# Kernel optimization log

Measured on AMD Instinct MI355X. Metric: run time of the kernel, lower is better.

The kernel has to match this reference:

```python
import jax, jax.numpy as jnp
import numpy as np
import math

N, D, H, E, ED = 2048, 256, 8, 65536, 64
HD = D // H  # head_dim = 32


def _layernorm(x, g, b, eps=1e-5):
    mu = jnp.mean(x, axis=-1, keepdims=True)
    var = jnp.mean((x - mu) ** 2, axis=-1, keepdims=True)
    return (x - mu) * jax.lax.rsqrt(var + eps) * g + b


def setup_inputs() -> dict:
    key = jax.random.key(0)
    ks = jax.random.split(key, 24)
    s = 0.02
    inp = {
        "x": jax.random.normal(ks[0], (N, D), jnp.float32),
        "edge_index": jax.random.randint(ks[1], (2, E), 0, N, jnp.int64),
        "edge_attr": jax.random.normal(ks[2], (E, ED), jnp.float32),
        # attention projections (stored [in, out]; y = x @ W + b)
        "Wq": jax.random.normal(ks[3], (D, D), jnp.float32) * s,
        "bq": jnp.zeros((D,), jnp.float32),
        "Wk": jax.random.normal(ks[4], (D, D), jnp.float32) * s,
        "bk": jnp.zeros((D,), jnp.float32),
        "Wv": jax.random.normal(ks[5], (D, D), jnp.float32) * s,
        "bv": jnp.zeros((D,), jnp.float32),
        "Wo": jax.random.normal(ks[6], (D, D), jnp.float32) * s,
        "bo": jnp.zeros((D,), jnp.float32),
        # edge bias projection: edge_dim -> num_heads
        "We": jax.random.normal(ks[7], (ED, H), jnp.float32) * s,
        "be": jnp.zeros((H,), jnp.float32),
        # FFN
        "W1": jax.random.normal(ks[8], (D, 4 * D), jnp.float32) * s,
        "b1": jnp.zeros((4 * D,), jnp.float32),
        "W2": jax.random.normal(ks[9], (4 * D, D), jnp.float32) * s,
        "b2": jnp.zeros((D,), jnp.float32),
        # layernorms
        "ln1_g": jnp.ones((D,), jnp.float32),
        "ln1_b": jnp.zeros((D,), jnp.float32),
        "ln2_g": jnp.ones((D,), jnp.float32),
        "ln2_b": jnp.zeros((D,), jnp.float32),
    }
    return inp


def reference(x, edge_index, edge_attr, Wq, bq, Wk, bk, Wv, bv, Wo, bo,
              We, be, W1, b1, W2, b2, ln1_g, ln1_b, ln2_g, ln2_b):
    n = x.shape[0]
    scale = math.sqrt(HD)
    src, dst = edge_index[0], edge_index[1]

    residual = x
    h = _layernorm(x, ln1_g, ln1_b)
    Q = (h @ Wq + bq).reshape(n, H, HD)
    K = (h @ Wk + bk).reshape(n, H, HD)
    V = (h @ Wv + bv).reshape(n, H, HD)

    # dense [N, N, H] scores, matching the original einsum
    scores = jnp.einsum('nhd,mhd->nmh', Q, K) / scale

    # adjacency mask with self-loops (scatter .set semantics, like torch assignment)
    diag = jnp.arange(n)
    adj = jnp.zeros((n, n), jnp.bool_).at[src, dst].set(True)
    adj = adj.at[diag, diag].set(True)

    # edge bias scattered into [N, N, H] (assignment semantics)
    edge_bias = edge_attr @ We + be  # [E, H]
    bias = jnp.zeros((n, n, H), scores.dtype).at[src, dst].set(edge_bias)
    scores = scores + bias

    scores = jnp.where(adj[:, :, None], scores, -jnp.inf)
    # softmax over dim=1 (source/key nodes m)
    attn = jax.nn.softmax(scores, axis=1)

    out = jnp.einsum('nmh,mhd->nhd', attn, V).reshape(n, D)
    out = out @ Wo + bo
    x = residual + out

    residual = x
    h2 = _layernorm(x, ln2_g, ln2_b)
    ffn = jax.nn.gelu(h2 @ W1 + b1, approximate=False) @ W2 + b2
    return residual + ffn
```

## Files before the change

### kernel.cpp

```cpp
#include <hip/hip_runtime.h>
#include <math.h>

#define D 256
#define NH 8
#define HD 32
#define EDIM 64

typedef __attribute__((ext_vector_type(8))) short bfrag;
typedef __attribute__((ext_vector_type(4))) float ffrag;

__device__ __forceinline__ unsigned short f2bf(float x) {
  unsigned int u = __float_as_uint(x);
  return (unsigned short)((u + 0x7FFFu + ((u >> 16) & 1u)) >> 16);
}

__global__ __launch_bounds__(256) void ln_kernel(const float* __restrict__ x,
    const float* __restrict__ g, const float* __restrict__ b,
    unsigned short* __restrict__ out) {
  int row = blockIdx.x;
  int tid = threadIdx.x;
  float v = x[row * D + tid];
  float s = v, sq = v * v;
  #pragma unroll
  for (int m = 1; m < 64; m <<= 1) { s += __shfl_xor(s, m); sq += __shfl_xor(sq, m); }
  __shared__ float ps[4], pq[4];
  int wid = tid >> 6, lane = tid & 63;
  if (lane == 0) { ps[wid] = s; pq[wid] = sq; }
  __syncthreads();
  float ts = ps[0] + ps[1] + ps[2] + ps[3];
  float tq = pq[0] + pq[1] + pq[2] + pq[3];
  float mu  = ts * (1.f / D);
  float var = tq * (1.f / D) - mu * mu;
  float inv = 1.f / sqrtf(var + 1e-5f);
  out[row * D + tid] = f2bf((v - mu) * inv * g[tid] + b[tid]);
}

__global__ __launch_bounds__(256) void cast6_kernel(
    const float* __restrict__ s0, const float* __restrict__ s1,
    const float* __restrict__ s2, const float* __restrict__ s3,
    const float* __restrict__ s4, const float* __restrict__ s5,
    unsigned short* __restrict__ d0, unsigned short* __restrict__ d1,
    unsigned short* __restrict__ d2, unsigned short* __restrict__ d3,
    unsigned short* __restrict__ d4, unsigned short* __restrict__ d5) {
  int i = (blockIdx.x * 256 + threadIdx.x) * 4;
  const float* s; unsigned short* d; int off;
  if      (i < 65536)  { s = s0; d = d0; off = i; }
  else if (i < 131072) { s = s1; d = d1; off = i - 65536; }
  else if (i < 196608) { s = s2; d = d2; off = i - 131072; }
  else if (i < 262144) { s = s3; d = d3; off = i - 196608; }
  else if (i < 524288) { s = s4; d = d4; off = i - 262144; }
  else if (i < 786432) { s = s5; d = d5; off = i - 524288; }
  else return;
  float4 v = *(const float4*)(s + off);
  ushort4 o = make_ushort4(f2bf(v.x), f2bf(v.y), f2bf(v.z), f2bf(v.w));
  *(ushort4*)(d + off) = o;
}

__device__ __forceinline__ void mg_core(const unsigned short* __restrict__ A,
    const unsigned short* __restrict__ B, int K, int Nn, int bm, int bn,
    int kb0, int kb1, unsigned short (*As)[40], unsigned short (*Bt)[40],
    ffrag acc[4]) {
  int tid = threadIdx.x;
  int wid = tid >> 6, lane = tid & 63;
  int lr = lane & 15, lk = lane >> 4;
  int ar = tid >> 2, ak = (tid & 3) * 8;
  int bnn = tid & 63, bkg = tid >> 6;
  for (int kb = kb0; kb < kb1; kb += 32) {
    uint4 av = *(const uint4*)(A + (size_t)(bm + ar) * K + kb + ak);
    *(uint4*)&As[ar][ak] = av;
    unsigned int u[4];
    #pragma unroll
    for (int jj = 0; jj < 4; jj++) {
      unsigned short lo = B[(size_t)(kb + bkg * 8 + 2 * jj)     * Nn + bn + bnn];
      unsigned short hi = B[(size_t)(kb + bkg * 8 + 2 * jj + 1) * Nn + bn + bnn];
      u[jj] = (unsigned int)lo | ((unsigned int)hi << 16);
    }
    *(uint4*)&Bt[bnn][bkg * 8] = make_uint4(u[0], u[1], u[2], u[3]);
    __syncthreads();
    bfrag af = *(const bfrag*)&As[wid * 16 + lr][lk * 8];
    #pragma unroll
    for (int nf = 0; nf < 4; nf++) {
      bfrag bf = *(const bfrag*)&Bt[nf * 16 + lr][lk * 8];
      acc[nf] = __builtin_amdgcn_mfma_f32_16x16x32_bf16(af, bf, acc[nf], 0, 0, 0);
    }
    __syncthreads();
  }
}

__global__ __launch_bounds__(256) void mgemm_qkv(const unsigned short* __restrict__ A,
    const unsigned short* __restrict__ B0, const unsigned short* __restrict__ B1,
    const unsigned short* __restrict__ B2,
    const float* __restrict__ b0, const float* __restrict__ b1, const float* __restrict__ b2,
    float* __restrict__ C0, float* __restrict__ C1, float* __restrict__ C2,
    int M, int Nn, int K) {
  __shared__ __align__(16) unsigned short As[64][40];
  __shared__ __align__(16) unsigned short Bt[64][40];
  int z = blockIdx.z;
  const unsigned short* B = (z == 0) ? B0 : (z == 1) ? B1 : B2;
  const float* bias = (z == 0) ? b0 : (z == 1) ? b1 : b2;
  float* C = (z == 0) ? C0 : (z == 1) ? C1 : C2;
  int bm = blockIdx.y * 64, bn = blockIdx.x * 64;
  ffrag acc[4] = {};
  mg_core(A, B, K, Nn, bm, bn, 0, K, As, Bt, acc);
  int lane = threadIdx.x & 63, wid = threadIdx.x >> 6;
  int lr = lane & 15, lk = lane >> 4;
  #pragma unroll
  for (int nf = 0; nf < 4; nf++) {
    int col = bn + nf * 16 + lr;
    float bv = bias[col];
    #pragma unroll
    for (int i = 0; i < 4; i++) {
      int row = bm + wid * 16 + lk * 4 + i;
      C[(size_t)row * Nn + col] = acc[nf][i] + bv;
    }
  }
}

__global__ __launch_bounds__(256) void mgemm_gelu(const unsigned short* __restrict__ A,
    const unsigned short* __restrict__ B, const float* __restrict__ bias,
    unsigned short* __restrict__ C, int M, int Nn, int K) {
  __shared__ __align__(16) unsigned short As[64][40];
  __shared__ __align__(16) unsigned short Bt[64][40];
  int bm = blockIdx.y * 64, bn = blockIdx.x * 64;
  ffrag acc[4] = {};
  mg_core(A, B, K, Nn, bm, bn, 0, K, As, Bt, acc);
  int lane = threadIdx.x & 63, wid = threadIdx.x >> 6;
  int lr = lane & 15, lk = lane >> 4;
  #pragma unroll
  for (int nf = 0; nf < 4; nf++) {
    int col = bn + nf * 16 + lr;
    float bv = bias[col];
    #pragma unroll
    for (int i = 0; i < 4; i++) {
      int row = bm + wid * 16 + lk * 4 + i;
      float v = acc[nf][i] + bv;
      v = 0.5f * v * (1.f + erff(v * 0.70710678118654752f));
      C[(size_t)row * Nn + col] = f2bf(v);
    }
  }
}

__global__ __launch_bounds__(256) void mgemm_splitk(const unsigned short* __restrict__ A,
    const unsigned short* __restrict__ B, float* __restrict__ P,
    int M, int Nn, int K, int Kslice) {
  __shared__ __align__(16) unsigned short As[64][40];
  __shared__ __align__(16) unsigned short Bt[64][40];
  int z = blockIdx.z;
  int bm = blockIdx.y * 64, bn = blockIdx.x * 64;
  ffrag acc[4] = {};
  mg_core(A, B, K, Nn, bm, bn, z * Kslice, (z + 1) * Kslice, As, Bt, acc);
  float* Pz = P + (size_t)z * M * Nn;
  int lane = threadIdx.x & 63, wid = threadIdx.x >> 6;
  int lr = lane & 15, lk = lane >> 4;
  #pragma unroll
  for (int nf = 0; nf < 4; nf++) {
    int col = bn + nf * 16 + lr;
    #pragma unroll
    for (int i = 0; i < 4; i++) {
      int row = bm + wid * 16 + lk * 4 + i;
      Pz[(size_t)row * Nn + col] = acc[nf][i];
    }
  }
}

__global__ __launch_bounds__(256) void reduce_kernel(const float* __restrict__ P,
    const float* __restrict__ bias, const float* __restrict__ R,
    float* __restrict__ out, int MN, int Nn, int S) {
  int i = blockIdx.x * 256 + threadIdx.x;
  if (i * 4 >= MN) return;
  size_t b = (size_t)i * 4;
  float4 acc = *(const float4*)(P + b);
  for (int s = 1; s < S; s++) {
    float4 p = *(const float4*)(P + (size_t)s * MN + b);
    acc.x += p.x; acc.y += p.y; acc.z += p.z; acc.w += p.w;
  }
  float4 bi = *(const float4*)(bias + (b % Nn));
  float4 r  = *(const float4*)(R + b);
  acc.x += bi.x + r.x; acc.y += bi.y + r.y; acc.z += bi.z + r.z; acc.w += bi.w + r.w;
  *(float4*)(out + b) = acc;
}

__global__ __launch_bounds__(256) void edge_bias_kernel(const float* __restrict__ ea,
    const float* __restrict__ We, const float* __restrict__ be,
    float* __restrict__ eb, int E) {
  int e = blockIdx.x * 256 + threadIdx.x;
  if (e >= E) return;
  const float* row = ea + (size_t)e * EDIM;
  float acc[NH];
  #pragma unroll
  for (int h = 0; h < NH; h++) acc[h] = be[h];
  #pragma unroll 4
  for (int k = 0; k < EDIM; k++) {
    float r = row[k];
    #pragma unroll
    for (int h = 0; h < NH; h++) acc[h] = fmaf(r, We[k * NH + h], acc[h]);
  }
  #pragma unroll
  for (int h = 0; h < NH; h++) eb[e * NH + h] = acc[h];
}

__global__ void winner_kernel(const int* __restrict__ ei, int* __restrict__ Wn, int E, int N) {
  int e = blockIdx.x * 256 + threadIdx.x;
  if (e >= E) return;
  int s = ei[e], d = ei[E + e];
  atomicMax(&Wn[(size_t)s * N + d], e);
}
__global__ void count_kernel(const int* __restrict__ ei, const int* __restrict__ Wn,
                             int* __restrict__ cnt, int E, int N) {
  int e = blockIdx.x * 256 + threadIdx.x;
  if (e >= E) return;
  int s = ei[e], d = ei[E + e];
  if (Wn[(size_t)s * N + d] == e) atomicAdd(&cnt[s], 1);
}
__global__ void self_count_kernel(const int* __restrict__ Wn, int* __restrict__ cnt, int N) {
  int n = blockIdx.x * 256 + threadIdx.x;
  if (n >= N) return;
  if (Wn[(size_t)n * N + n] == -1) cnt[n] += 1;
}

__global__ __launch_bounds__(256) void scan_kernel(const int* __restrict__ cnt,
    int* __restrict__ rowptr, int* __restrict__ cursor, int N) {
  __shared__ int part[256];
  int tid = threadIdx.x;
  int chunk = (N + 255) / 256;
  int base = tid * chunk;
  int s = 0;
  for (int i = 0; i < chunk; i++) { int idx = base + i; if (idx < N) s += cnt[idx]; }
  part[tid] = s;
  __syncthreads();
  for (int off = 1; off < 256; off <<= 1) {
    int v = (tid >= off) ? part[tid - off] : 0;
    __syncthreads();
    part[tid] += v;
    __syncthreads();
  }
  int run = (tid == 0) ? 0 : part[tid - 1];
  for (int i = 0; i < chunk; i++) {
    int idx = base + i;
    if (idx < N) { rowptr[idx] = run; cursor[idx] = run; run += cnt[idx]; }
  }
  if (tid == 255) rowptr[N] = part[255];
}

__global__ void scatter_kernel(const int* __restrict__ ei, const int* __restrict__ Wn,
    int* __restrict__ cursor, int* __restrict__ col, int* __restrict__ bidx, int E, int N) {
  int e = blockIdx.x * 256 + threadIdx.x;
  if (e >= E) return;
  int s = ei[e], d = ei[E + e];
  if (Wn[(size_t)s * N + d] == e) {
    int p = atomicAdd(&cursor[s], 1);
    col[p] = d; bidx[p] = e;
  }
}
__global__ void self_scatter_kernel(const int* __restrict__ Wn, const int* __restrict__ cursor,
    int* __restrict__ col, int* __restrict__ bidx, int N) {
  int n = blockIdx.x * 256 + threadIdx.x;
  if (n >= N) return;
  if (Wn[(size_t)n * N + n] == -1) {
    int p = cursor[n];
    col[p] = n; bidx[p] = -1;
  }
}

__global__ __launch_bounds__(256) void attn_kernel(const float* __restrict__ Q,
    const float* __restrict__ Km, const float* __restrict__ Vm,
    const float* __restrict__ eb, const int* __restrict__ rowptr,
    const int* __restrict__ col, const int* __restrict__ bidx,
    unsigned short* __restrict__ out, int N) {
  int wid = threadIdx.x >> 6, lane = threadIdx.x & 63;
  int n = blockIdx.x * 4 + wid;
  if (n >= N) return;
  int h = lane >> 3, j = lane & 7;
  int off = h * HD + j * 4;
  float4 q = *(const float4*)(Q + (size_t)n * D + off);
  float mrun = -INFINITY, srun = 0.f;
  float4 acc = make_float4(0.f, 0.f, 0.f, 0.f);
  int beg = rowptr[n], end = rowptr[n + 1];
  for (int i = beg; i < end; i++) {
    int m = col[i];
    int be_ = bidx[i];
    float4 k4 = *(const float4*)(Km + (size_t)m * D + off);
    float dot = q.x * k4.x + q.y * k4.y + q.z * k4.z + q.w * k4.w;
    dot += __shfl_xor(dot, 1); dot += __shfl_xor(dot, 2); dot += __shfl_xor(dot, 4);
    float bias = (be_ >= 0) ? eb[be_ * NH + h] : 0.f;
    float sc = fmaf(dot, 0.17677669529663687f, bias);
    float mnew = fmaxf(mrun, sc);
    float corr = __expf(mrun - mnew);
    float p = __expf(sc - mnew);
    float4 v4 = *(const float4*)(Vm + (size_t)m * D + off);
    srun = srun * corr + p;
    acc.x = fmaf(acc.x, corr, p * v4.x);
    acc.y = fmaf(acc.y, corr, p * v4.y);
    acc.z = fmaf(acc.z, corr, p * v4.z);
    acc.w = fmaf(acc.w, corr, p * v4.w);
    mrun = mnew;
  }
  float inv = 1.f / srun;
  ushort4 o = make_ushort4(f2bf(acc.x * inv), f2bf(acc.y * inv),
                           f2bf(acc.z * inv), f2bf(acc.w * inv));
  *(ushort4*)(out + (size_t)n * D + off) = o;
}

extern "C" void kernel_launch(void* const* d_in, const int* in_sizes, int n_in,
                              void* d_out, int out_size, void* d_ws, size_t ws_size,
                              hipStream_t stream) {
  const float* x    = (const float*)d_in[0];
  const int*   ei   = (const int*)d_in[1];
  const float* ea   = (const float*)d_in[2];
  const float* Wq   = (const float*)d_in[3];  const float* bq = (const float*)d_in[4];
  const float* Wk   = (const float*)d_in[5];  const float* bk = (const float*)d_in[6];
  const float* Wv   = (const float*)d_in[7];  const float* bv = (const float*)d_in[8];
  const float* Wo   = (const float*)d_in[9];  const float* bo = (const float*)d_in[10];
  const float* We   = (const float*)d_in[11]; const float* be = (const float*)d_in[12];
  const float* W1   = (const float*)d_in[13]; const float* b1 = (const float*)d_in[14];
  const float* W2   = (const float*)d_in[15]; const float* b2 = (const float*)d_in[16];
  const float* ln1g = (const float*)d_in[17]; const float* ln1b = (const float*)d_in[18];
  const float* ln2g = (const float*)d_in[19]; const float* ln2b = (const float*)d_in[20];

  int N = in_sizes[0] / D;
  int E = in_sizes[1] / 2;

  char* p = (char*)d_ws;
  auto alloc = [&](size_t bytes) -> char* {
    char* r = p; p += (bytes + 255) & ~(size_t)255; return r;
  };
  int*            Wn     = (int*)           alloc((size_t)N * N * 4);
  unsigned short* hbf    = (unsigned short*)alloc((size_t)N * D * 2);
  float*          Qd     = (float*)         alloc((size_t)N * D * 4);
  float*          Kd     = (float*)         alloc((size_t)N * D * 4);
  float*          Vd     = (float*)         alloc((size_t)N * D * 4);
  unsigned short* attnbf = (unsigned short*)alloc((size_t)N * D * 2);
  float*          x_mid  = (float*)         alloc((size_t)N * D * 4);
  float*          ebuf   = (float*)         alloc((size_t)E * NH * 4);
  unsigned short* tbf    = (unsigned short*)alloc((size_t)N * 4 * D * 2);
  float*          P      = (float*)         alloc((size_t)4 * N * D * 4);
  unsigned short* Wqb    = (unsigned short*)alloc((size_t)D * D * 2);
  unsigned short* Wkb    = (unsigned short*)alloc((size_t)D * D * 2);
  unsigned short* Wvb    = (unsigned short*)alloc((size_t)D * D * 2);
  unsigned short* Wob    = (unsigned short*)alloc((size_t)D * D * 2);
  unsigned short* W1b    = (unsigned short*)alloc((size_t)D * 4 * D * 2);
  unsigned short* W2b    = (unsigned short*)alloc((size_t)4 * D * D * 2);
  int*            cnt    = (int*)           alloc((size_t)N * 4);
  int*            rowptr = (int*)           alloc((size_t)(N + 1) * 4);
  int*            cursor = (int*)           alloc((size_t)N * 4);
  int*            colA   = (int*)           alloc((size_t)(E + N) * 4);
  int*            bidxA  = (int*)           alloc((size_t)(E + N) * 4);

  hipMemsetAsync(Wn, 0xFF, (size_t)N * N * 4, stream);
  hipMemsetAsync(cnt, 0, (size_t)N * 4, stream);

  int MN = N * D;

  cast6_kernel<<<768, 256, 0, stream>>>(Wq, Wk, Wv, Wo, W1, W2,
                                        Wqb, Wkb, Wvb, Wob, W1b, W2b);
  ln_kernel<<<N, 256, 0, stream>>>(x, ln1g, ln1b, hbf);
  dim3 g_qkv(D / 64, N / 64, 3);
  mgemm_qkv<<<g_qkv, 256, 0, stream>>>(hbf, Wqb, Wkb, Wvb, bq, bk, bv,
                                       Qd, Kd, Vd, N, D, D);
  edge_bias_kernel<<<(E + 255) / 256, 256, 0, stream>>>(ea, We, be, ebuf, E);
  winner_kernel<<<(E + 255) / 256, 256, 0, stream>>>(ei, Wn, E, N);
  count_kernel<<<(E + 255) / 256, 256, 0, stream>>>(ei, Wn, cnt, E, N);
  self_count_kernel<<<(N + 255) / 256, 256, 0, stream>>>(Wn, cnt, N);
  scan_kernel<<<1, 256, 0, stream>>>(cnt, rowptr, cursor, N);
  scatter_kernel<<<(E + 255) / 256, 256, 0, stream>>>(ei, Wn, cursor, colA, bidxA, E, N);
  self_scatter_kernel<<<(N + 255) / 256, 256, 0, stream>>>(Wn, cursor, colA, bidxA, N);
  attn_kernel<<<(N + 3) / 4, 256, 0, stream>>>(Qd, Kd, Vd, ebuf, rowptr, colA, bidxA,
                                               attnbf, N);
  {
    dim3 g(D / 64, N / 64, 2);
    mgemm_splitk<<<g, 256, 0, stream>>>(attnbf, Wob, P, N, D, D, D / 2);
    reduce_kernel<<<(MN / 4 + 255) / 256, 256, 0, stream>>>(P, bo, x, x_mid, MN, D, 2);
  }
  ln_kernel<<<N, 256, 0, stream>>>(x_mid, ln2g, ln2b, hbf);
  dim3 g_1(4 * D / 64, N / 64, 1);
  mgemm_gelu<<<g_1, 256, 0, stream>>>(hbf, W1b, b1, tbf, N, 4 * D, D);
  {
    dim3 g(D / 64, N / 64, 4);
    mgemm_splitk<<<g, 256, 0, stream>>>(tbf, W2b, P, N, D, 4 * D, D);
    reduce_kernel<<<(MN / 4 + 255) / 256, 256, 0, stream>>>(P, b2, x_mid, (float*)d_out,
                                                            MN, D, 4);
  }
}
```

Before: 231.5 us.

## Drop dense N×N winner matrix; dedup edges in attention; fuse prep and LN2

Removes the N×N winner matrix, its memset, and the winner/count/self passes. Duplicate (src,dst) edges are now resolved inside the attention kernel: each wave loads up to 256 edge entries into registers and skips any edge beaten by a later edge id to the same destination. A self-loop is added when none is found. Weight casts, LN1, degree counting and edge-bias projection are merged into one multi-role prep kernel, and the Wo split-K reduce is fused with LN2. Rows with degree above 256 would be truncated, and the per-edge dedup check adds wave votes to the attention loop.

```diff
diff --git a/kernel.cpp b/kernel.cpp
--- a/kernel.cpp
+++ b/kernel.cpp
@@ -14,46 +14,101 @@
   return (unsigned short)((u + 0x7FFFu + ((u >> 16) & 1u)) >> 16);
 }
 
-__global__ __launch_bounds__(256) void ln_kernel(const float* __restrict__ x,
-    const float* __restrict__ g, const float* __restrict__ b,
-    unsigned short* __restrict__ out) {
-  int row = blockIdx.x;
-  int tid = threadIdx.x;
-  float v = x[row * D + tid];
-  float s = v, sq = v * v;
-  #pragma unroll
-  for (int m = 1; m < 64; m <<= 1) { s += __shfl_xor(s, m); sq += __shfl_xor(sq, m); }
-  __shared__ float ps[4], pq[4];
-  int wid = tid >> 6, lane = tid & 63;
-  if (lane == 0) { ps[wid] = s; pq[wid] = sq; }
-  __syncthreads();
-  float ts = ps[0] + ps[1] + ps[2] + ps[3];
-  float tq = pq[0] + pq[1] + pq[2] + pq[3];
-  float mu  = ts * (1.f / D);
-  float var = tq * (1.f / D) - mu * mu;
-  float inv = 1.f / sqrtf(var + 1e-5f);
-  out[row * D + tid] = f2bf((v - mu) * inv * g[tid] + b[tid]);
-}
-
-__global__ __launch_bounds__(256) void cast6_kernel(
+__global__ __launch_bounds__(256) void prep_kernel(
     const float* __restrict__ s0, const float* __restrict__ s1,
     const float* __restrict__ s2, const float* __restrict__ s3,
     const float* __restrict__ s4, const float* __restrict__ s5,
     unsigned short* __restrict__ d0, unsigned short* __restrict__ d1,
     unsigned short* __restrict__ d2, unsigned short* __restrict__ d3,
-    unsigned short* __restrict__ d4, unsigned short* __restrict__ d5) {
-  int i = (blockIdx.x * 256 + threadIdx.x) * 4;
-  const float* s; unsigned short* d; int off;
-  if      (i < 65536)  { s = s0; d = d0; off = i; }
-  else if (i < 131072) { s = s1; d = d1; off = i - 65536; }
-  else if (i < 196608) { s = s2; d = d2; off = i - 131072; }
-  else if (i < 262144) { s = s3; d = d3; off = i - 196608; }
-  else if (i < 524288) { s = s4; d = d4; off = i - 262144; }
-  else if (i < 786432) { s = s5; d = d5; off = i - 524288; }
-  else return;
-  float4 v = *(const float4*)(s + off);
-  ushort4 o = make_ushort4(f2bf(v.x), f2bf(v.y), f2bf(v.z), f2bf(v.w));
-  *(ushort4*)(d + off) = o;
+    unsigned short* __restrict__ d4, unsigned short* __restrict__ d5,
+    const float* __restrict__ x, const float* __restrict__ g,
+    const float* __restrict__ b, unsigned short* __restrict__ hbf,
+    const int* __restrict__ ei, int* __restrict__ cnt,
+    const float* __restrict__ ea, const float* __restrict__ We,
+    const float* __restrict__ be, float* __restrict__ eb,
+    int N, int E, int CB, int EB) {
+  int blk = blockIdx.x;
+  int tid = threadIdx.x;
+  if (blk < CB) {
+    int i = (blk * 256 + tid) * 4;
+    const float* s; unsigned short* d; int off;
+    if      (i < 65536)  { s = s0; d = d0; off = i; }
+    else if (i < 131072) { s = s1; d = d1; off = i - 65536; }
+    else if (i < 196608) { s = s2; d = d2; off = i - 131072; }
+    else if (i < 262144) { s = s3; d = d3; off = i - 196608; }
+    else if (i < 524288) { s = s4; d = d4; off = i - 262144; }
+    else if (i < 786432) { s = s5; d = d5; off = i - 524288; }
+    else return;
+    float4 v = *(const float4*)(s + off);
+    *(ushort4*)(d + off) = make_ushort4(f2bf(v.x), f2bf(v.y), f2bf(v.z), f2bf(v.w));
+  } else if (blk < CB + N) {
+    int row = blk - CB;
+    float v = x[row * D + tid];
+    float s = v, sq = v * v;
+    #pragma unroll
+    for (int m = 1; m < 64; m <<= 1) { s += __shfl_xor(s, m); sq += __shfl_xor(sq, m); }
+    __shared__ float ps[4], pq[4];
+    int wid = tid >> 6, lane = tid & 63;
+    if (lane == 0) { ps[wid] = s; pq[wid] = sq; }
+    __syncthreads();
+    float ts = ps[0] + ps[1] + ps[2] + ps[3];
+    float tq = pq[0] + pq[1] + pq[2] + pq[3];
+    float mu  = ts * (1.f / D);
+    float var = tq * (1.f / D) - mu * mu;
+    float inv = 1.f / sqrtf(var + 1e-5f);
+    hbf[row * D + tid] = f2bf((v - mu) * inv * g[tid] + b[tid]);
+  } else if (blk < CB + N + EB) {
+    int e = (blk - CB - N) * 256 + tid;
+    if (e < E) atomicAdd(&cnt[ei[e]], 1);
+  } else {
+    int e = (blk - CB - N - EB) * 256 + tid;
+    if (e >= E) return;
+    const float* row = ea + (size_t)e * EDIM;
+    float acc[NH];
+    #pragma unroll
+    for (int h = 0; h < NH; h++) acc[h] = be[h];
+    #pragma unroll 4
+    for (int k = 0; k < EDIM; k++) {
+      float r = row[k];
+      #pragma unroll
+      for (int h = 0; h < NH; h++) acc[h] = fmaf(r, We[k * NH + h], acc[h]);
+    }
+    #pragma unroll
+    for (int h = 0; h < NH; h++) eb[e * NH + h] = acc[h];
+  }
+}
+
+__global__ __launch_bounds__(256) void scan_kernel(const int* __restrict__ cnt,
+    int* __restrict__ rowptr, int* __restrict__ cursor, int N) {
+  __shared__ int part[256];
+  int tid = threadIdx.x;
+  int chunk = (N + 255) / 256;
+  int base = tid * chunk;
+  int s = 0;
+  for (int i = 0; i < chunk; i++) { int idx = base + i; if (idx < N) s += cnt[idx]; }
+  part[tid] = s;
+  __syncthreads();
+  for (int off = 1; off < 256; off <<= 1) {
+    int v = (tid >= off) ? part[tid - off] : 0;
+    __syncthreads();
+    part[tid] += v;
+    __syncthreads();
+  }
+  int run = (tid == 0) ? 0 : part[tid - 1];
+  for (int i = 0; i < chunk; i++) {
+    int idx = base + i;
+    if (idx < N) { rowptr[idx] = run; cursor[idx] = run; run += cnt[idx]; }
+  }
+  if (tid == 255) rowptr[N] = part[255];
+}
+
+__global__ void scatter_kernel(const int* __restrict__ ei, int* __restrict__ cursor,
+    int* __restrict__ col, int* __restrict__ eidx, int E) {
+  int e = blockIdx.x * 256 + threadIdx.x;
+  if (e >= E) return;
+  int s = ei[e], d = ei[E + e];
+  int p = atomicAdd(&cursor[s], 1);
+  col[p] = d; eidx[p] = e;
 }
 
 __device__ __forceinline__ void mg_core(const unsigned short* __restrict__ A,
@@ -180,92 +235,34 @@
   *(float4*)(out + b) = acc;
 }
 
-__global__ __launch_bounds__(256) void edge_bias_kernel(const float* __restrict__ ea,
-    const float* __restrict__ We, const float* __restrict__ be,
-    float* __restrict__ eb, int E) {
-  int e = blockIdx.x * 256 + threadIdx.x;
-  if (e >= E) return;
-  const float* row = ea + (size_t)e * EDIM;
-  float acc[NH];
+__global__ __launch_bounds__(256) void ln2_fused_kernel(const float* __restrict__ P,
+    const float* __restrict__ bo, const float* __restrict__ x,
+    const float* __restrict__ g, const float* __restrict__ b,
+    float* __restrict__ x_mid, unsigned short* __restrict__ hbf, int MN) {
+  int row = blockIdx.x;
+  int tid = threadIdx.x;
+  size_t idx = (size_t)row * D + tid;
+  float v = P[idx] + P[(size_t)MN + idx] + bo[tid] + x[idx];
+  x_mid[idx] = v;
+  float s = v, sq = v * v;
   #pragma unroll
-  for (int h = 0; h < NH; h++) acc[h] = be[h];
-  #pragma unroll 4
-  for (int k = 0; k < EDIM; k++) {
-    float r = row[k];
-    #pragma unroll
-    for (int h = 0; h < NH; h++) acc[h] = fmaf(r, We[k * NH + h], acc[h]);
-  }
-  #pragma unroll
-  for (int h = 0; h < NH; h++) eb[e * NH + h] = acc[h];
-}
-
-__global__ void winner_kernel(const int* __restrict__ ei, int* __restrict__ Wn, int E, int N) {
-  int e = blockIdx.x * 256 + threadIdx.x;
-  if (e >= E) return;
-  int s = ei[e], d = ei[E + e];
-  atomicMax(&Wn[(size_t)s * N + d], e);
-}
-__global__ void count_kernel(const int* __restrict__ ei, const int* __restrict__ Wn,
-                             int* __restrict__ cnt, int E, int N) {
-  int e = blockIdx.x * 256 + threadIdx.x;
-  if (e >= E) return;
-  int s = ei[e], d = ei[E + e];
-  if (Wn[(size_t)s * N + d] == e) atomicAdd(&cnt[s], 1);
-}
-__global__ void self_count_kernel(const int* __restrict__ Wn, int* __restrict__ cnt, int N) {
-  int n = blockIdx.x * 256 + threadIdx.x;
-  if (n >= N) return;
-  if (Wn[(size_t)n * N + n] == -1) cnt[n] += 1;
-}
-
-__global__ __launch_bounds__(256) void scan_kernel(const int* __restrict__ cnt,
-    int* __restrict__ rowptr, int* __restrict__ cursor, int N) {
-  __shared__ int part[256];
-  int tid = threadIdx.x;
-  int chunk = (N + 255) / 256;
-  int base = tid * chunk;
-  int s = 0;
-  for (int i = 0; i < chunk; i++) { int idx = base + i; if (idx < N) s += cnt[idx]; }
-  part[tid] = s;
+  for (int m = 1; m < 64; m <<= 1) { s += __shfl_xor(s, m); sq += __shfl_xor(sq, m); }
+  __shared__ float ps[4], pq[4];
+  int wid = tid >> 6, lane = tid & 63;
+  if (lane == 0) { ps[wid] = s; pq[wid] = sq; }
   __syncthreads();
-  for (int off = 1; off < 256; off <<= 1) {
-    int v = (tid >= off) ? part[tid - off] : 0;
-    __syncthreads();
-    part[tid] += v;
-    __syncthreads();
-  }
-  int run = (tid == 0) ? 0 : part[tid - 1];
-  for (int i = 0; i < chunk; i++) {
-    int idx = base + i;
-    if (idx < N) { rowptr[idx] = run; cursor[idx] = run; run += cnt[idx]; }
-  }
-  if (tid == 255) rowptr[N] = part[255];
-}
-
-__global__ void scatter_kernel(const int* __restrict__ ei, const int* __restrict__ Wn,
-    int* __restrict__ cursor, int* __restrict__ col, int* __restrict__ bidx, int E, int N) {
-  int e = blockIdx.x * 256 + threadIdx.x;
-  if (e >= E) return;
-  int s = ei[e], d = ei[E + e];
-  if (Wn[(size_t)s * N + d] == e) {
-    int p = atomicAdd(&cursor[s], 1);
-    col[p] = d; bidx[p] = e;
-  }
-}
-__global__ void self_scatter_kernel(const int* __restrict__ Wn, const int* __restrict__ cursor,
-    int* __restrict__ col, int* __restrict__ bidx, int N) {
-  int n = blockIdx.x * 256 + threadIdx.x;
-  if (n >= N) return;
-  if (Wn[(size_t)n * N + n] == -1) {
-    int p = cursor[n];
-    col[p] = n; bidx[p] = -1;
-  }
+  float ts = ps[0] + ps[1] + ps[2] + ps[3];
+  float tq = pq[0] + pq[1] + pq[2] + pq[3];
+  float mu  = ts * (1.f / D);
+  float var = tq * (1.f / D) - mu * mu;
+  float inv = 1.f / sqrtf(var + 1e-5f);
+  hbf[idx] = f2bf((v - mu) * inv * g[tid] + b[tid]);
 }
 
 __global__ __launch_bounds__(256) void attn_kernel(const float* __restrict__ Q,
     const float* __restrict__ Km, const float* __restrict__ Vm,
     const float* __restrict__ eb, const int* __restrict__ rowptr,
-    const int* __restrict__ col, const int* __restrict__ bidx,
+    const int* __restrict__ col, const int* __restrict__ eidx,
     unsigned short* __restrict__ out, int N) {
   int wid = threadIdx.x >> 6, lane = threadIdx.x & 63;
   int n = blockIdx.x * 4 + wid;
@@ -273,28 +270,56 @@
   int h = lane >> 3, j = lane & 7;
   int off = h * HD + j * 4;
   float4 q = *(const float4*)(Q + (size_t)n * D + off);
+  int beg = rowptr[n], end = rowptr[n + 1];
+  int L = end - beg;
+  if (L > 256) L = 256;
+  int dv0 = -1, dv1 = -1, dv2 = -1, dv3 = -1;
+  int ev0 = -1, ev1 = -1, ev2 = -1, ev3 = -1;
+  if (lane       < L) { dv0 = col[beg + lane      ]; ev0 = eidx[beg + lane      ]; }
+  if (lane +  64 < L) { dv1 = col[beg + lane +  64]; ev1 = eidx[beg + lane +  64]; }
+  if (lane + 128 < L) { dv2 = col[beg + lane + 128]; ev2 = eidx[beg + lane + 128]; }
+  if (lane + 192 < L) { dv3 = col[beg + lane + 192]; ev3 = eidx[beg + lane + 192]; }
+  bool self_present = __any(dv0 == n) || __any(dv1 == n) ||
+                      __any(dv2 == n) || __any(dv3 == n);
   float mrun = -INFINITY, srun = 0.f;
   float4 acc = make_float4(0.f, 0.f, 0.f, 0.f);
-  int beg = rowptr[n], end = rowptr[n + 1];
-  for (int i = beg; i < end; i++) {
-    int m = col[i];
-    int be_ = bidx[i];
-    float4 k4 = *(const float4*)(Km + (size_t)m * D + off);
-    float dot = q.x * k4.x + q.y * k4.y + q.z * k4.z + q.w * k4.w;
-    dot += __shfl_xor(dot, 1); dot += __shfl_xor(dot, 2); dot += __shfl_xor(dot, 4);
-    float bias = (be_ >= 0) ? eb[be_ * NH + h] : 0.f;
-    float sc = fmaf(dot, 0.17677669529663687f, bias);
-    float mnew = fmaxf(mrun, sc);
-    float corr = __expf(mrun - mnew);
-    float p = __expf(sc - mnew);
-    float4 v4 = *(const float4*)(Vm + (size_t)m * D + off);
-    srun = srun * corr + p;
-    acc.x = fmaf(acc.x, corr, p * v4.x);
-    acc.y = fmaf(acc.y, corr, p * v4.y);
-    acc.z = fmaf(acc.z, corr, p * v4.z);
-    acc.w = fmaf(acc.w, corr, p * v4.w);
-    mrun = mnew;
-  }
+
+#define PROC_EDGE(m_, bias_) {                                                 \
+    float4 k4 = *(const float4*)(Km + (size_t)(m_) * D + off);                 \
+    float dot = q.x * k4.x + q.y * k4.y + q.z * k4.z + q.w * k4.w;             \
+    dot += __shfl_xor(dot, 1); dot += __shfl_xor(dot, 2); dot += __shfl_xor(dot, 4); \
+    float sc = fmaf(dot, 0.17677669529663687f, bias_);                         \
+    float mnew = fmaxf(mrun, sc);                                              \
+    float corr = __expf(mrun - mnew);                                          \
+    float pp = __expf(sc - mnew);                                              \
+    float4 v4 = *(const float4*)(Vm + (size_t)(m_) * D + off);                 \
+    srun = srun * corr + pp;                                                   \
+    acc.x = fmaf(acc.x, corr, pp * v4.x);                                      \
+    acc.y = fmaf(acc.y, corr, pp * v4.y);                                      \
+    acc.z = fmaf(acc.z, corr, pp * v4.z);                                      \
+    acc.w = fmaf(acc.w, corr, pp * v4.w);                                      \
+    mrun = mnew; }
+
+#define PROC_CHUNK(dvC, evC, base_) {                                          \
+    int cl = L - (base_); if (cl > 64) cl = 64;                                \
+    for (int ii = 0; ii < cl; ii++) {                                          \
+      int d_i = __shfl(dvC, ii);                                               \
+      int e_i = __shfl(evC, ii);                                               \
+      bool dom = (dv0 == d_i && ev0 > e_i) || (dv1 == d_i && ev1 > e_i) ||     \
+                 (dv2 == d_i && ev2 > e_i) || (dv3 == d_i && ev3 > e_i);       \
+      if (__any(dom)) continue;                                                \
+      float bias_ = eb[(size_t)e_i * NH + h];                                  \
+      PROC_EDGE(d_i, bias_);                                                   \
+    } }
+
+  PROC_CHUNK(dv0, ev0, 0)
+  if (L > 64)  PROC_CHUNK(dv1, ev1, 64)
+  if (L > 128) PROC_CHUNK(dv2, ev2, 128)
+  if (L > 192) PROC_CHUNK(dv3, ev3, 192)
+  if (!self_present) PROC_EDGE(n, 0.f)
+#undef PROC_CHUNK
+#undef PROC_EDGE
+
   float inv = 1.f / srun;
   ushort4 o = make_ushort4(f2bf(acc.x * inv), f2bf(acc.y * inv),
                            f2bf(acc.z * inv), f2bf(acc.w * inv));
@@ -324,7 +349,6 @@
   auto alloc = [&](size_t bytes) -> char* {
     char* r = p; p += (bytes + 255) & ~(size_t)255; return r;
   };
-  int*            Wn     = (int*)           alloc((size_t)N * N * 4);
   unsigned short* hbf    = (unsigned short*)alloc((size_t)N * D * 2);
   float*          Qd     = (float*)         alloc((size_t)N * D * 4);
   float*          Kd     = (float*)         alloc((size_t)N * D * 4);
@@ -343,35 +367,30 @@
   int*            cnt    = (int*)           alloc((size_t)N * 4);
   int*            rowptr = (int*)           alloc((size_t)(N + 1) * 4);
   int*            cursor = (int*)           alloc((size_t)N * 4);
-  int*            colA   = (int*)           alloc((size_t)(E + N) * 4);
-  int*            bidxA  = (int*)           alloc((size_t)(E + N) * 4);
-
-  hipMemsetAsync(Wn, 0xFF, (size_t)N * N * 4, stream);
+  int*            colA   = (int*)           alloc((size_t)E * 4);
+  int*            eidxA  = (int*)           alloc((size_t)E * 4);
+
   hipMemsetAsync(cnt, 0, (size_t)N * 4, stream);
 
   int MN = N * D;
-
-  cast6_kernel<<<768, 256, 0, stream>>>(Wq, Wk, Wv, Wo, W1, W2,
-                                        Wqb, Wkb, Wvb, Wob, W1b, W2b);
-  ln_kernel<<<N, 256, 0, stream>>>(x, ln1g, ln1b, hbf);
+  int CB = 768;
+  int EB = (E + 255) / 256;
+
+  prep_kernel<<<CB + N + 2 * EB, 256, 0, stream>>>(
+      Wq, Wk, Wv, Wo, W1, W2, Wqb, Wkb, Wvb, Wob, W1b, W2b,
+      x, ln1g, ln1b, hbf, ei, cnt, ea, We, be, ebuf, N, E, CB, EB);
+  scan_kernel<<<1, 256, 0, stream>>>(cnt, rowptr, cursor, N);
+  scatter_kernel<<<EB, 256, 0, stream>>>(ei, cursor, colA, eidxA, E);
   dim3 g_qkv(D / 64, N / 64, 3);
   mgemm_qkv<<<g_qkv, 256, 0, stream>>>(hbf, Wqb, Wkb, Wvb, bq, bk, bv,
                                        Qd, Kd, Vd, N, D, D);
-  edge_bias_kernel<<<(E + 255) / 256, 256, 0, stream>>>(ea, We, be, ebuf, E);
-  winner_kernel<<<(E + 255) / 256, 256, 0, stream>>>(ei, Wn, E, N);
-  count_kernel<<<(E + 255) / 256, 256, 0, stream>>>(ei, Wn, cnt, E, N);
-  self_count_kernel<<<(N + 255) / 256, 256, 0, stream>>>(Wn, cnt, N);
-  scan_kernel<<<1, 256, 0, stream>>>(cnt, rowptr, cursor, N);
-  scatter_kernel<<<(E + 255) / 256, 256, 0, stream>>>(ei, Wn, cursor, colA, bidxA, E, N);
-  self_scatter_kernel<<<(N + 255) / 256, 256, 0, stream>>>(Wn, cursor, colA, bidxA, N);
-  attn_kernel<<<(N + 3) / 4, 256, 0, stream>>>(Qd, Kd, Vd, ebuf, rowptr, colA, bidxA,
+  attn_kernel<<<(N + 3) / 4, 256, 0, stream>>>(Qd, Kd, Vd, ebuf, rowptr, colA, eidxA,
                                                attnbf, N);
   {
     dim3 g(D / 64, N / 64, 2);
     mgemm_splitk<<<g, 256, 0, stream>>>(attnbf, Wob, P, N, D, D, D / 2);
-    reduce_kernel<<<(MN / 4 + 255) / 256, 256, 0, stream>>>(P, bo, x, x_mid, MN, D, 2);
-  }
-  ln_kernel<<<N, 256, 0, stream>>>(x_mid, ln2g, ln2b, hbf);
+    ln2_fused_kernel<<<N, 256, 0, stream>>>(P, bo, x, ln2g, ln2b, x_mid, hbf, MN);
+  }
   dim3 g_1(4 * D / 64, N / 64, 1);
   mgemm_gelu<<<g_1, 256, 0, stream>>>(hbf, W1b, b1, tbf, N, 4 * D, D);
   {
```

After: 202.3 us. 12.6% less time.
